# Optimization experiments

Measured on AMD Instinct MI355X. Metric: run time of the kernel, lower is better.

## Reference

```python
import jax, jax.numpy as jnp
import numpy as np

M0, M1 = 32, 16          # multiplicities of 0e (scalars) and 1o (vectors)
FEAT = M0 + 3 * M1       # 80
WNUM = M0*M0 + M1*M1 + M0*M1 + M1*M0  # 2304 per-edge TP weights
N_NODES, N_EDGES, N_RBF, HID = 10000, 160000, 50, 64
EPS = 1e-5
INV_SQRT3 = 1.0 / np.sqrt(3.0)
# per-path normalization: 1/sqrt(num_paths_to_output * mul_in)
A_P1 = 1.0 / np.sqrt(2.0 * M0)   # 0e x 0e -> 0e
A_P4 = 1.0 / np.sqrt(2.0 * M1)   # 1o x 1o -> 0e
A_P2 = 1.0 / np.sqrt(2.0 * M1)   # 1o x 0e -> 1o
A_P3 = 1.0 / np.sqrt(2.0 * M0)   # 0e x 1o -> 1o


def setup_inputs() -> dict:
    key = jax.random.key(0)
    ks = jax.random.split(key, 12)
    def lin(k, fi, fo):
        return jax.random.normal(k, (fi, fo), jnp.float32) / np.sqrt(fi)
    return dict(
        h=jax.random.normal(ks[0], (N_NODES, FEAT), jnp.float32),
        edge_index=jax.random.randint(ks[1], (2, N_EDGES), 0, N_NODES),
        edge_sh=jax.random.normal(ks[2], (N_EDGES, 4), jnp.float32),
        edge_features=jax.random.normal(ks[3], (N_EDGES, N_RBF), jnp.float32),
        W1e=lin(ks[4], N_RBF, HID), b1e=jnp.zeros(HID, jnp.float32),
        W2e=lin(ks[5], HID, HID), b2e=jnp.zeros(HID, jnp.float32),
        W3e=lin(ks[6], HID, WNUM) * 0.1, b3e=jnp.zeros(WNUM, jnp.float32),
        A0=jax.random.normal(ks[7], (M0, M0), jnp.float32),
        A1p=jax.random.normal(ks[8], (M1, M1), jnp.float32),
        bn_w0=jnp.ones(M0, jnp.float32), bn_b0=jnp.zeros(M0, jnp.float32),
        bn_w1=jnp.ones(M1, jnp.float32),
    )


def _forward(h, edge_index, edge_sh, edge_features,
             W1e, b1e, W2e, b2e, W3e, b3e, A0, A1p, bn_w0, bn_b0, bn_w1):
    N = h.shape[0]
    E = edge_sh.shape[0]
    src, dst = edge_index[0], edge_index[1]

    # ---- edge MLP -> per-edge tensor-product weights [E, WNUM] ----
    w = jax.nn.silu(edge_features @ W1e + b1e)
    w = jax.nn.silu(w @ W2e + b2e)
    w = w @ W3e + b3e
    o1 = M0 * M0
    o2 = o1 + M1 * M1
    o3 = o2 + M0 * M1
    w1 = w[:, :o1].reshape(E, M0, M0)     # 0e x 0e -> 0e
    w2 = w[:, o1:o2].reshape(E, M1, M1)   # 1o x 0e -> 1o
    w3 = w[:, o2:o3].reshape(E, M0, M1)   # 0e x 1o -> 1o
    w4 = w[:, o3:].reshape(E, M1, M0)     # 1o x 1o -> 0e

    # ---- gather source node features ----
    s0 = h[src, :M0]                         # [E, M0]
    s1 = h[src, M0:].reshape(E, M1, 3)       # [E, M1, 3]
    y0 = edge_sh[:, 0]                       # [E]
    y1 = edge_sh[:, 1:4]                     # [E, 3]

    # ---- fully connected tensor product with per-edge weights ----
    # scalar output: 0e x 0e -> 0e  and  1o x 1o -> 0e (dot / sqrt(3))
    dot11 = jnp.einsum('eui,ei->eu', s1, y1) * INV_SQRT3      # [E, M1]
    m0 = (A_P1 * jnp.einsum('eu,euw->ew', s0 * y0[:, None], w1)
          + A_P4 * jnp.einsum('eu,euw->ew', dot11, w4))       # [E, M0]
    # vector output: 1o x 0e -> 1o  and  0e x 1o -> 1o
    m1 = (A_P2 * jnp.einsum('eui,euw->ewi', s1 * y0[:, None, None], w2)
          + A_P3 * jnp.einsum('eu,ei,euw->ewi', s0, y1, w3))  # [E, M1, 3]
    messages = jnp.concatenate([m0, m1.reshape(E, 3 * M1)], axis=1)  # [E, FEAT]

    # ---- scatter-mean aggregation to destination nodes ----
    agg = jax.ops.segment_sum(messages, dst, num_segments=N)
    cnt = jax.ops.segment_sum(jnp.ones((E,), messages.dtype), dst, num_segments=N)
    agg = agg / jnp.maximum(cnt, 1.0)[:, None]

    # ---- equivariant self-interaction (per-l linear mixing) ----
    self0 = (h[:, :M0] @ A0) / np.sqrt(M0)
    h1 = h[:, M0:].reshape(N, M1, 3)
    self1 = jnp.einsum('nui,uw->nwi', h1, A1p) / np.sqrt(M1)
    out = agg + jnp.concatenate([self0, self1.reshape(N, 3 * M1)], axis=1)

    # ---- equivariant batch norm (layer mode) ----
    x0 = out[:, :M0]
    x1 = out[:, M0:].reshape(N, M1, 3)
    mu = x0.mean(axis=0)
    var = x0.var(axis=0)
    x0n = (x0 - mu) * jax.lax.rsqrt(var + EPS) * bn_w0 + bn_b0
    nrm2 = (x1 ** 2).sum(axis=-1).mean(axis=0)               # [M1]
    x1n = x1 * (jax.lax.rsqrt(nrm2 + EPS) * bn_w1)[None, :, None]
    out = jnp.concatenate([x0n, x1n.reshape(N, 3 * M1)], axis=1)

    # ---- residual (irreps_in == irreps_out) ----
    return out + h


def reference(h, edge_index, edge_sh, edge_features,
              W1e, b1e, W2e, b2e, W3e, b3e, A0, A1p, bn_w0, bn_b0, bn_w1):
    return _forward(h, edge_index, edge_sh, edge_features,
                    W1e, b1e, W2e, b2e, W3e, b3e, A0, A1p, bn_w0, bn_b0, bn_w1)
```

## Files before the change

### kernel.cpp

```cpp
#include <hip/hip_runtime.h>
#include <math.h>

#define NN 10000
#define NE 160000
#define NRBF 50
#define WNUM 2304
#define EPSV 1e-5f

#define A_P1 0.125f
#define A_P2 0.17677669529663687f
#define A_P3 0.125f
#define A_P4 0.17677669529663687f
#define INV_SQRT3 0.5773502691896258f
#define INV_SQRT_M0 0.17677669529663687f
#define INV_SQRT_M1 0.25f

typedef __attribute__((ext_vector_type(8))) short bf16x8;
typedef __attribute__((ext_vector_type(4))) float f32x4;
typedef __attribute__((ext_vector_type(4))) int i32x4;

#define MFMA16(a, b, c) __builtin_amdgcn_mfma_f32_16x16x32_bf16(a, b, c, 0, 0, 0)

__device__ __forceinline__ short f2bf(float x) {
  unsigned u = __float_as_uint(x);
  unsigned r = (u + 0x7fffu + ((u >> 16) & 1u)) >> 16;
  return (short)r;
}

__global__ void prep_weights(const float* __restrict__ W1, const float* __restrict__ W2,
                             const float* __restrict__ W3, short* __restrict__ W1P,
                             short* __restrict__ W2P, short* __restrict__ W3P) {
  int s = blockIdx.x * 256 + threadIdx.x;
  if (s < WNUM * 64) {
    int t = s >> 10, r = s & 1023;
    int ch = r >> 9, l = (r >> 3) & 63, kk = r & 7;
    int row = t * 16 + (l & 15);
    int k = ((l >> 4) << 3) + (ch << 5) + kk;
    W3P[s] = f2bf(W3[k * WNUM + row]);
  } else if (s < WNUM * 64 + 4096) {
    int s2 = s - WNUM * 64;
    int t = s2 >> 10, r = s2 & 1023;
    int ch = r >> 9, l = (r >> 3) & 63, kk = r & 7;
    int row = t * 16 + (l & 15);
    int k = ((l >> 4) << 3) + (ch << 5) + kk;
    W1P[s2] = f2bf(k < NRBF ? W1[k * 64 + row] : 0.f);
  } else if (s < WNUM * 64 + 8192) {
    int s2 = s - WNUM * 64 - 4096;
    int t = s2 >> 10, r = s2 & 1023;
    int ch = r >> 9, l = (r >> 3) & 63, kk = r & 7;
    int row = t * 16 + (l & 15);
    int k = ((l >> 4) << 3) + (ch << 5) + kk;
    W2P[s2] = f2bf(W2[k * 64 + row]);
  }
}

#define TILE_V(JT, V)                                         \
  {                                                           \
    const short* wb = W3P + ((JT) << 10) + (l << 3);          \
    bf16x8 b0 = *(const bf16x8*)wb;                           \
    bf16x8 b1f = *(const bf16x8*)(wb + 512);                  \
    float bias = b3[((JT) << 4) + lr];                        \
    f32x4 d = {bias, bias, bias, bias};                       \
    d = MFMA16(a0, b0, d);                                    \
    V = MFMA16(a1, b1f, d);                                   \
  }

__global__ __launch_bounds__(256, 3) void edge_kernel(
    const float* __restrict__ h, const int* __restrict__ eidx,
    const float* __restrict__ esh, const float* __restrict__ ef,
    const short* __restrict__ W1P, const float* __restrict__ b1,
    const short* __restrict__ W2P, const float* __restrict__ b2,
    const short* __restrict__ W3P, const float* __restrict__ b3,
    float* __restrict__ agg, float* __restrict__ cnt) {
  __shared__ short buf0[64 * 72];
  __shared__ short h1s[64 * 72];
  __shared__ float a0s[32 * 64];
  __shared__ float s0c[32 * 64];
  __shared__ float cYs[3 * 16 * 64];
  __shared__ float d4s[16 * 64];
  __shared__ float y1s[3 * 64];
  __shared__ float b1s[64], b2s[64];
  __shared__ int dsts[64];

  const int tid = threadIdx.x;
  const int e0 = blockIdx.x * 64;

  for (int idx = tid; idx < 64 * 64; idx += 256) {
    int e = idx >> 6, k = idx & 63;
    float v = (k < NRBF) ? ef[(long)(e0 + e) * NRBF + k] : 0.f;
    buf0[e * 72 + k] = f2bf(v);
  }
  if (tid < 64) { b1s[tid] = b1[tid]; b2s[tid] = b2[tid]; }
  {
    int e = tid >> 2, q = tid & 3;
    int ge = e0 + e;
    int src = eidx[ge];
    float y0 = esh[ge * 4 + 0];
    float y1x = esh[ge * 4 + 1], y1y = esh[ge * 4 + 2], y1z = esh[ge * 4 + 3];
    const float* hs = h + (long)src * 80;
    for (int u = q; u < 32; u += 4) {
      float s = hs[u];
      a0s[u * 64 + e] = A_P1 * y0 * s;
      s0c[u * 64 + e] = A_P3 * s;
    }
    for (int u = q; u < 16; u += 4) {
      float sx = hs[32 + u * 3], sy = hs[33 + u * 3], sz = hs[34 + u * 3];
      cYs[(0 * 16 + u) * 64 + e] = A_P2 * y0 * sx;
      cYs[(1 * 16 + u) * 64 + e] = A_P2 * y0 * sy;
      cYs[(2 * 16 + u) * 64 + e] = A_P2 * y0 * sz;
      d4s[u * 64 + e] = A_P4 * INV_SQRT3 * (sx * y1x + sy * y1y + sz * y1z);
    }
    if (q == 0) {
      y1s[0 * 64 + e] = y1x; y1s[1 * 64 + e] = y1y; y1s[2 * 64 + e] = y1z;
      dsts[e] = eidx[NE + ge];
    }
  }
  __syncthreads();

  const int wid = tid >> 6, l = tid & 63;
  const int er = wid * 16;
  const int lr = l & 15, lg = l >> 4;
  const int row4 = er + lg * 4;

  {
    bf16x8 a0 = *(const bf16x8*)&buf0[(er + lr) * 72 + lg * 8];
    bf16x8 a1 = *(const bf16x8*)&buf0[(er + lr) * 72 + 32 + lg * 8];
#pragma unroll
    for (int jt = 0; jt < 4; ++jt) {
      const short* wb = W1P + (jt << 10) + (l << 3);
      bf16x8 b0 = *(const bf16x8*)wb;
      bf16x8 b1f = *(const bf16x8*)(wb + 512);
      float bias = b1s[jt * 16 + lr];
      f32x4 d = {bias, bias, bias, bias};
      d = MFMA16(a0, b0, d);
      d = MFMA16(a1, b1f, d);
#pragma unroll
      for (int r = 0; r < 4; ++r) {
        float x = d[r];
        x = x / (1.f + __expf(-x));
        h1s[(row4 + r) * 72 + jt * 16 + lr] = f2bf(x);
      }
    }
  }
  __syncthreads();

  {
    bf16x8 a0 = *(const bf16x8*)&h1s[(er + lr) * 72 + lg * 8];
    bf16x8 a1 = *(const bf16x8*)&h1s[(er + lr) * 72 + 32 + lg * 8];
#pragma unroll
    for (int jt = 0; jt < 4; ++jt) {
      const short* wb = W2P + (jt << 10) + (l << 3);
      bf16x8 b0 = *(const bf16x8*)wb;
      bf16x8 b1f = *(const bf16x8*)(wb + 512);
      float bias = b2s[jt * 16 + lr];
      f32x4 d = {bias, bias, bias, bias};
      d = MFMA16(a0, b0, d);
      d = MFMA16(a1, b1f, d);
#pragma unroll
      for (int r = 0; r < 4; ++r) {
        float x = d[r];
        x = x / (1.f + __expf(-x));
        buf0[(row4 + r) * 72 + jt * 16 + lr] = f2bf(x);
      }
    }
  }
  __syncthreads();

  bf16x8 a0 = *(const bf16x8*)&buf0[(er + lr) * 72 + lg * 8];
  bf16x8 a1 = *(const bf16x8*)&buf0[(er + lr) * 72 + 32 + lg * 8];
  f32x4 y1r0 = *(const f32x4*)&y1s[0 * 64 + row4];
  f32x4 y1r1 = *(const f32x4*)&y1s[1 * 64 + row4];
  f32x4 y1r2 = *(const f32x4*)&y1s[2 * 64 + row4];
  i32x4 dd = *(const i32x4*)&dsts[row4];

  f32x4 m0f0 = {0.f, 0.f, 0.f, 0.f}, m0f1 = {0.f, 0.f, 0.f, 0.f};
  f32x4 m1f0 = {0.f, 0.f, 0.f, 0.f}, m1f1 = {0.f, 0.f, 0.f, 0.f},
        m1f2 = {0.f, 0.f, 0.f, 0.f};

#pragma unroll 2
  for (int jp = 0; jp < 32; ++jp) {
    f32x4 c = *(const f32x4*)&a0s[jp * 64 + row4];
    f32x4 v, v2;
    TILE_V(jp * 2, v);
    TILE_V(jp * 2 + 1, v2);
#pragma unroll
    for (int r = 0; r < 4; ++r) {
      m0f0[r] += c[r] * v[r];
      m0f1[r] += c[r] * v2[r];
    }
  }

#pragma unroll 4
  for (int u = 0; u < 16; ++u) {
    f32x4 v;
    TILE_V(64 + u, v);
    f32x4 c0 = *(const f32x4*)&cYs[(0 * 16 + u) * 64 + row4];
    f32x4 c1 = *(const f32x4*)&cYs[(1 * 16 + u) * 64 + row4];
    f32x4 c2 = *(const f32x4*)&cYs[(2 * 16 + u) * 64 + row4];
#pragma unroll
    for (int r = 0; r < 4; ++r) {
      m1f0[r] += c0[r] * v[r];
      m1f1[r] += c1[r] * v[r];
      m1f2[r] += c2[r] * v[r];
    }
  }

#pragma unroll 4
  for (int u = 0; u < 32; ++u) {
    f32x4 v;
    TILE_V(80 + u, v);
    f32x4 c = *(const f32x4*)&s0c[u * 64 + row4];
#pragma unroll
    for (int r = 0; r < 4; ++r) {
      float t = c[r] * v[r];
      m1f0[r] += t * y1r0[r];
      m1f1[r] += t * y1r1[r];
      m1f2[r] += t * y1r2[r];
    }
  }

#pragma unroll 2
  for (int up = 0; up < 16; ++up) {
    f32x4 c = *(const f32x4*)&d4s[up * 64 + row4];
    f32x4 v, v2;
    TILE_V(112 + up * 2, v);
    TILE_V(112 + up * 2 + 1, v2);
#pragma unroll
    for (int r = 0; r < 4; ++r) {
      m0f0[r] += c[r] * v[r];
      m0f1[r] += c[r] * v2[r];
    }
  }

#pragma unroll
  for (int r = 0; r < 4; ++r) {
    float* base = agg + (long)dd[r] * 80;
    atomicAdd(base + lr, m0f0[r]);
    atomicAdd(base + 16 + lr, m0f1[r]);
    atomicAdd(base + 32 + lr * 3 + 0, m1f0[r]);
    atomicAdd(base + 32 + lr * 3 + 1, m1f1[r]);
    atomicAdd(base + 32 + lr * 3 + 2, m1f2[r]);
  }
  if (tid < 64) atomicAdd(cnt + dsts[tid], 1.0f);
}

__global__ __launch_bounds__(256) void node_a(
    const float* __restrict__ h, const float* __restrict__ A0,
    const float* __restrict__ A1p, const float* __restrict__ agg,
    const float* __restrict__ cnt, float* __restrict__ outpre,
    float* __restrict__ stats) {
  __shared__ float redw[4][80];
  const int tid = threadIdx.x;
  const int wid = tid >> 6, l = tid & 63;
  const int n = blockIdx.x * 256 + tid;
  float x0[32], x1[48];
#pragma unroll
  for (int w = 0; w < 32; w++) x0[w] = 0.f;
#pragma unroll
  for (int c = 0; c < 48; c++) x1[c] = 0.f;
  if (n < NN) {
    const float* hr = h + (long)n * 80;
    const float* ar = agg + (long)n * 80;
    float inv = 1.f / fmaxf(cnt[n], 1.f);
#pragma unroll 1
    for (int u = 0; u < 32; u++) {
      float hu = hr[u];
#pragma unroll
      for (int w = 0; w < 32; w++) x0[w] += hu * A0[u * 32 + w];
    }
#pragma unroll
    for (int w = 0; w < 32; w++) x0[w] = x0[w] * INV_SQRT_M0 + ar[w] * inv;
#pragma unroll 1
    for (int u = 0; u < 16; u++) {
      float a = hr[32 + u * 3], b_ = hr[33 + u * 3], c_ = hr[34 + u * 3];
#pragma unroll
      for (int w = 0; w < 16; w++) {
        float Aw = A1p[u * 16 + w];
        x1[w * 3 + 0] += a * Aw;
        x1[w * 3 + 1] += b_ * Aw;
        x1[w * 3 + 2] += c_ * Aw;
      }
    }
#pragma unroll
    for (int c = 0; c < 48; c++) x1[c] = x1[c] * INV_SQRT_M1 + ar[32 + c] * inv;
    float* opr = outpre + (long)n * 80;
#pragma unroll
    for (int w = 0; w < 32; w++) opr[w] = x0[w];
#pragma unroll
    for (int c = 0; c < 48; c++) opr[32 + c] = x1[c];
  }
#pragma unroll 1
  for (int c = 0; c < 32; ++c) {
    float s = x0[c];
#pragma unroll
    for (int m = 32; m >= 1; m >>= 1) s += __shfl_xor(s, m, 64);
    if (l == 0) redw[wid][c] = s;
  }
#pragma unroll 1
  for (int c = 0; c < 32; ++c) {
    float v = x0[c];
    float s = v * v;
#pragma unroll
    for (int m = 32; m >= 1; m >>= 1) s += __shfl_xor(s, m, 64);
    if (l == 0) redw[wid][32 + c] = s;
  }
#pragma unroll 1
  for (int u = 0; u < 16; ++u) {
    float s = x1[u * 3] * x1[u * 3] + x1[u * 3 + 1] * x1[u * 3 + 1] +
              x1[u * 3 + 2] * x1[u * 3 + 2];
#pragma unroll
    for (int m = 32; m >= 1; m >>= 1) s += __shfl_xor(s, m, 64);
    if (l == 0) redw[wid][64 + u] = s;
  }
  __syncthreads();
  if (tid < 80)
    atomicAdd(&stats[tid],
              redw[0][tid] + redw[1][tid] + redw[2][tid] + redw[3][tid]);
}

__global__ void node_b(const float* __restrict__ outpre, const float* __restrict__ stats,
                       const float* __restrict__ bnw0, const float* __restrict__ bnb0,
                       const float* __restrict__ bnw1, const float* __restrict__ h,
                       float* __restrict__ out) {
  int idx = blockIdx.x * 256 + threadIdx.x;
  if (idx >= NN * 80) return;
  int c = idx % 80;
  float v = outpre[idx];
  const float invN = 1.f / NN;
  float o;
  if (c < 32) {
    float mu = stats[c] * invN;
    float var = stats[32 + c] * invN - mu * mu;
    o = (v - mu) * rsqrtf(var + EPSV) * bnw0[c] + bnb0[c];
  } else {
    int u = (c - 32) / 3;
    float nr = stats[64 + u] * invN;
    o = v * rsqrtf(nr + EPSV) * bnw1[u];
  }
  out[idx] = o + h[idx];
}

extern "C" void kernel_launch(void* const* d_in, const int* in_sizes, int n_in,
                              void* d_out, int out_size, void* d_ws, size_t ws_size,
                              hipStream_t stream) {
  const float* h    = (const float*)d_in[0];
  const int*   eidx = (const int*)d_in[1];
  const float* esh  = (const float*)d_in[2];
  const float* ef   = (const float*)d_in[3];
  const float* W1   = (const float*)d_in[4];
  const float* b1   = (const float*)d_in[5];
  const float* W2   = (const float*)d_in[6];
  const float* b2   = (const float*)d_in[7];
  const float* W3   = (const float*)d_in[8];
  const float* b3   = (const float*)d_in[9];
  const float* A0   = (const float*)d_in[10];
  const float* A1p  = (const float*)d_in[11];
  const float* bnw0 = (const float*)d_in[12];
  const float* bnb0 = (const float*)d_in[13];
  const float* bnw1 = (const float*)d_in[14];
  float* out = (float*)d_out;

  float* ws = (float*)d_ws;
  float* agg    = ws;
  float* cnt    = ws + 800000;
  float* stats  = ws + 810000;
  float* outpre = ws + 810080;
  short* W3P    = (short*)(ws + 1610080);
  short* W1P    = W3P + WNUM * 64;
  short* W2P    = W1P + 4096;

  hipMemsetAsync(agg, 0, (size_t)810080 * sizeof(float), stream);

  prep_weights<<<(WNUM * 64 + 8192 + 255) / 256, 256, 0, stream>>>(W1, W2, W3, W1P,
                                                                   W2P, W3P);
  edge_kernel<<<NE / 64, 256, 0, stream>>>(h, eidx, esh, ef, W1P, b1, W2P, b2, W3P, b3,
                                           agg, cnt);
  node_a<<<(NN + 255) / 256, 256, 0, stream>>>(h, A0, A1p, agg, cnt, outpre, stats);
  node_b<<<(NN * 80 + 255) / 256, 256, 0, stream>>>(outpre, stats, bnw0, bnb0, bnw1, h,
                                                    out);
}
```

Measured before the change: 234.7 us.

## Split W3 tiles across wave halves, reuse each B fragment for two edge groups

The third-layer weight tiles are now split between two wave halves. Each wave computes two 16-edge row groups against each loaded W3 fragment, which halves the global weight loads per MFMA. The y0 factor is pulled out of the per-u coefficients and applied after accumulation, which shrinks the shared coefficient arrays into one buffer. The partial sums of the two halves are combined through shared memory with extra barriers. This raises register pressure and adds a reduction step, but cuts redundant weight traffic.

```diff
diff --git a/kernel.cpp b/kernel.cpp
--- a/kernel.cpp
+++ b/kernel.cpp
@@ -54,15 +54,18 @@
   }
 }
 
-#define TILE_V(JT, V)                                         \
+#define TILE_V2(TL, V0, V1)                                   \
   {                                                           \
-    const short* wb = W3P + ((JT) << 10) + (l << 3);          \
+    const short* wb = WB + ((TL) << 10) + (l << 3);           \
     bf16x8 b0 = *(const bf16x8*)wb;                           \
     bf16x8 b1f = *(const bf16x8*)(wb + 512);                  \
-    float bias = b3[((JT) << 4) + lr];                        \
-    f32x4 d = {bias, bias, bias, bias};                       \
-    d = MFMA16(a0, b0, d);                                    \
-    V = MFMA16(a1, b1f, d);                                   \
+    float bias = B3[((TL) << 4) + lr];                        \
+    f32x4 d0 = {bias, bias, bias, bias};                      \
+    f32x4 d1 = {bias, bias, bias, bias};                      \
+    d0 = MFMA16(aA0, b0, d0);                                 \
+    d1 = MFMA16(aB0, b0, d1);                                 \
+    V0 = MFMA16(aA1, b1f, d0);                                \
+    V1 = MFMA16(aB1, b1f, d1);                                \
   }
 
 __global__ __launch_bounds__(256, 3) void edge_kernel(
@@ -74,11 +77,8 @@
     float* __restrict__ agg, float* __restrict__ cnt) {
   __shared__ short buf0[64 * 72];
   __shared__ short h1s[64 * 72];
-  __shared__ float a0s[32 * 64];
-  __shared__ float s0c[32 * 64];
-  __shared__ float cYs[3 * 16 * 64];
-  __shared__ float d4s[16 * 64];
-  __shared__ float y1s[3 * 64];
+  __shared__ float coef[6144];
+  __shared__ float y0s[64], y1s[192];
   __shared__ float b1s[64], b2s[64];
   __shared__ int dsts[64];
 
@@ -98,31 +98,27 @@
     float y0 = esh[ge * 4 + 0];
     float y1x = esh[ge * 4 + 1], y1y = esh[ge * 4 + 2], y1z = esh[ge * 4 + 3];
     const float* hs = h + (long)src * 80;
-    for (int u = q; u < 32; u += 4) {
-      float s = hs[u];
-      a0s[u * 64 + e] = A_P1 * y0 * s;
-      s0c[u * 64 + e] = A_P3 * s;
-    }
+    for (int u = q; u < 32; u += 4) coef[u * 64 + e] = A_P3 * hs[u];
     for (int u = q; u < 16; u += 4) {
       float sx = hs[32 + u * 3], sy = hs[33 + u * 3], sz = hs[34 + u * 3];
-      cYs[(0 * 16 + u) * 64 + e] = A_P2 * y0 * sx;
-      cYs[(1 * 16 + u) * 64 + e] = A_P2 * y0 * sy;
-      cYs[(2 * 16 + u) * 64 + e] = A_P2 * y0 * sz;
-      d4s[u * 64 + e] = A_P4 * INV_SQRT3 * (sx * y1x + sy * y1y + sz * y1z);
+      coef[2048 + (0 * 16 + u) * 64 + e] = A_P2 * sx;
+      coef[2048 + (1 * 16 + u) * 64 + e] = A_P2 * sy;
+      coef[2048 + (2 * 16 + u) * 64 + e] = A_P2 * sz;
+      coef[5120 + u * 64 + e] = A_P4 * INV_SQRT3 * (sx * y1x + sy * y1y + sz * y1z);
     }
     if (q == 0) {
-      y1s[0 * 64 + e] = y1x; y1s[1 * 64 + e] = y1y; y1s[2 * 64 + e] = y1z;
+      y0s[e] = y0;
+      y1s[e] = y1x; y1s[64 + e] = y1y; y1s[128 + e] = y1z;
       dsts[e] = eidx[NE + ge];
     }
   }
   __syncthreads();
 
   const int wid = tid >> 6, l = tid & 63;
-  const int er = wid * 16;
   const int lr = l & 15, lg = l >> 4;
-  const int row4 = er + lg * 4;
 
   {
+    const int er = wid * 16;
     bf16x8 a0 = *(const bf16x8*)&buf0[(er + lr) * 72 + lg * 8];
     bf16x8 a1 = *(const bf16x8*)&buf0[(er + lr) * 72 + 32 + lg * 8];
 #pragma unroll
@@ -138,13 +134,14 @@
       for (int r = 0; r < 4; ++r) {
         float x = d[r];
         x = x / (1.f + __expf(-x));
-        h1s[(row4 + r) * 72 + jt * 16 + lr] = f2bf(x);
+        h1s[(er + lg * 4 + r) * 72 + jt * 16 + lr] = f2bf(x);
       }
     }
   }
   __syncthreads();
 
   {
+    const int er = wid * 16;
     bf16x8 a0 = *(const bf16x8*)&h1s[(er + lr) * 72 + lg * 8];
     bf16x8 a1 = *(const bf16x8*)&h1s[(er + lr) * 72 + 32 + lg * 8];
 #pragma unroll
@@ -160,86 +157,172 @@
       for (int r = 0; r < 4; ++r) {
         float x = d[r];
         x = x / (1.f + __expf(-x));
-        buf0[(row4 + r) * 72 + jt * 16 + lr] = f2bf(x);
-      }
-    }
-  }
-  __syncthreads();
-
-  bf16x8 a0 = *(const bf16x8*)&buf0[(er + lr) * 72 + lg * 8];
-  bf16x8 a1 = *(const bf16x8*)&buf0[(er + lr) * 72 + 32 + lg * 8];
-  f32x4 y1r0 = *(const f32x4*)&y1s[0 * 64 + row4];
-  f32x4 y1r1 = *(const f32x4*)&y1s[1 * 64 + row4];
-  f32x4 y1r2 = *(const f32x4*)&y1s[2 * 64 + row4];
-  i32x4 dd = *(const i32x4*)&dsts[row4];
-
-  f32x4 m0f0 = {0.f, 0.f, 0.f, 0.f}, m0f1 = {0.f, 0.f, 0.f, 0.f};
-  f32x4 m1f0 = {0.f, 0.f, 0.f, 0.f}, m1f1 = {0.f, 0.f, 0.f, 0.f},
-        m1f2 = {0.f, 0.f, 0.f, 0.f};
-
+        buf0[(er + lg * 4 + r) * 72 + jt * 16 + lr] = f2bf(x);
+      }
+    }
+  }
+  __syncthreads();
+
+  const int gpair = wid & 1, half = wid >> 1;
+  const int g0 = gpair * 2;
+  const int rowA = g0 * 16, rowB = (g0 + 1) * 16;
+  const int r4A = rowA + lg * 4, r4B = rowB + lg * 4;
+
+  bf16x8 aA0 = *(const bf16x8*)&buf0[(rowA + lr) * 72 + lg * 8];
+  bf16x8 aA1 = *(const bf16x8*)&buf0[(rowA + lr) * 72 + 32 + lg * 8];
+  bf16x8 aB0 = *(const bf16x8*)&buf0[(rowB + lr) * 72 + lg * 8];
+  bf16x8 aB1 = *(const bf16x8*)&buf0[(rowB + lr) * 72 + 32 + lg * 8];
+  f32x4 y0A = *(const f32x4*)&y0s[r4A];
+  f32x4 y0B = *(const f32x4*)&y0s[r4B];
+
+  const short* WB = W3P + ((half * 72) << 10);
+  const float* B3 = b3 + half * 72 * 16;
+
+  f32x4 s0A = {0,0,0,0}, s1A = {0,0,0,0}, s0B = {0,0,0,0}, s1B = {0,0,0,0};
+  f32x4 mxA = {0,0,0,0}, myA = {0,0,0,0}, mzA = {0,0,0,0};
+  f32x4 mxB = {0,0,0,0}, myB = {0,0,0,0}, mzB = {0,0,0,0};
+
+  if (half == 0) {
 #pragma unroll 2
-  for (int jp = 0; jp < 32; ++jp) {
-    f32x4 c = *(const f32x4*)&a0s[jp * 64 + row4];
-    f32x4 v, v2;
-    TILE_V(jp * 2, v);
-    TILE_V(jp * 2 + 1, v2);
-#pragma unroll
-    for (int r = 0; r < 4; ++r) {
-      m0f0[r] += c[r] * v[r];
-      m0f1[r] += c[r] * v2[r];
-    }
-  }
-
-#pragma unroll 4
-  for (int u = 0; u < 16; ++u) {
-    f32x4 v;
-    TILE_V(64 + u, v);
-    f32x4 c0 = *(const f32x4*)&cYs[(0 * 16 + u) * 64 + row4];
-    f32x4 c1 = *(const f32x4*)&cYs[(1 * 16 + u) * 64 + row4];
-    f32x4 c2 = *(const f32x4*)&cYs[(2 * 16 + u) * 64 + row4];
-#pragma unroll
-    for (int r = 0; r < 4; ++r) {
-      m1f0[r] += c0[r] * v[r];
-      m1f1[r] += c1[r] * v[r];
-      m1f2[r] += c2[r] * v[r];
-    }
-  }
-
-#pragma unroll 4
-  for (int u = 0; u < 32; ++u) {
-    f32x4 v;
-    TILE_V(80 + u, v);
-    f32x4 c = *(const f32x4*)&s0c[u * 64 + row4];
-#pragma unroll
-    for (int r = 0; r < 4; ++r) {
-      float t = c[r] * v[r];
-      m1f0[r] += t * y1r0[r];
-      m1f1[r] += t * y1r1[r];
-      m1f2[r] += t * y1r2[r];
-    }
-  }
-
+    for (int u = 0; u < 32; ++u) {
+      f32x4 cA = *(const f32x4*)&coef[u * 64 + r4A];
+      f32x4 cB = *(const f32x4*)&coef[u * 64 + r4B];
+      f32x4 vA0, vB0, vA1, vB1;
+      TILE_V2(2 * u, vA0, vB0);
+      TILE_V2(2 * u + 1, vA1, vB1);
+#pragma unroll
+      for (int r = 0; r < 4; ++r) {
+        s0A[r] += cA[r] * vA0[r]; s1A[r] += cA[r] * vA1[r];
+        s0B[r] += cB[r] * vB0[r]; s1B[r] += cB[r] * vB1[r];
+      }
+    }
+#pragma unroll
+    for (int r = 0; r < 4; ++r) {
+      s0A[r] *= y0A[r]; s1A[r] *= y0A[r];
+      s0B[r] *= y0B[r]; s1B[r] *= y0B[r];
+    }
 #pragma unroll 2
-  for (int up = 0; up < 16; ++up) {
-    f32x4 c = *(const f32x4*)&d4s[up * 64 + row4];
-    f32x4 v, v2;
-    TILE_V(112 + up * 2, v);
-    TILE_V(112 + up * 2 + 1, v2);
-#pragma unroll
-    for (int r = 0; r < 4; ++r) {
-      m0f0[r] += c[r] * v[r];
-      m0f1[r] += c[r] * v2[r];
-    }
-  }
-
-#pragma unroll
-  for (int r = 0; r < 4; ++r) {
-    float* base = agg + (long)dd[r] * 80;
-    atomicAdd(base + lr, m0f0[r]);
-    atomicAdd(base + 16 + lr, m0f1[r]);
-    atomicAdd(base + 32 + lr * 3 + 0, m1f0[r]);
-    atomicAdd(base + 32 + lr * 3 + 1, m1f1[r]);
-    atomicAdd(base + 32 + lr * 3 + 2, m1f2[r]);
+    for (int u = 0; u < 8; ++u) {
+      f32x4 v0, v1;
+      TILE_V2(64 + u, v0, v1);
+      f32x4 cxA = *(const f32x4*)&coef[2048 + (0 * 16 + u) * 64 + r4A];
+      f32x4 cyA = *(const f32x4*)&coef[2048 + (1 * 16 + u) * 64 + r4A];
+      f32x4 czA = *(const f32x4*)&coef[2048 + (2 * 16 + u) * 64 + r4A];
+      f32x4 cxB = *(const f32x4*)&coef[2048 + (0 * 16 + u) * 64 + r4B];
+      f32x4 cyB = *(const f32x4*)&coef[2048 + (1 * 16 + u) * 64 + r4B];
+      f32x4 czB = *(const f32x4*)&coef[2048 + (2 * 16 + u) * 64 + r4B];
+#pragma unroll
+      for (int r = 0; r < 4; ++r) {
+        mxA[r] += cxA[r] * v0[r]; myA[r] += cyA[r] * v0[r]; mzA[r] += czA[r] * v0[r];
+        mxB[r] += cxB[r] * v1[r]; myB[r] += cyB[r] * v1[r]; mzB[r] += czB[r] * v1[r];
+      }
+    }
+#pragma unroll
+    for (int r = 0; r < 4; ++r) {
+      mxA[r] *= y0A[r]; myA[r] *= y0A[r]; mzA[r] *= y0A[r];
+      mxB[r] *= y0B[r]; myB[r] *= y0B[r]; mzB[r] *= y0B[r];
+    }
+  } else {
+#pragma unroll 2
+    for (int u = 8; u < 16; ++u) {
+      f32x4 v0, v1;
+      TILE_V2(u - 8, v0, v1);
+      f32x4 cxA = *(const f32x4*)&coef[2048 + (0 * 16 + u) * 64 + r4A];
+      f32x4 cyA = *(const f32x4*)&coef[2048 + (1 * 16 + u) * 64 + r4A];
+      f32x4 czA = *(const f32x4*)&coef[2048 + (2 * 16 + u) * 64 + r4A];
+      f32x4 cxB = *(const f32x4*)&coef[2048 + (0 * 16 + u) * 64 + r4B];
+      f32x4 cyB = *(const f32x4*)&coef[2048 + (1 * 16 + u) * 64 + r4B];
+      f32x4 czB = *(const f32x4*)&coef[2048 + (2 * 16 + u) * 64 + r4B];
+#pragma unroll
+      for (int r = 0; r < 4; ++r) {
+        mxA[r] += cxA[r] * v0[r]; myA[r] += cyA[r] * v0[r]; mzA[r] += czA[r] * v0[r];
+        mxB[r] += cxB[r] * v1[r]; myB[r] += cyB[r] * v1[r]; mzB[r] += czB[r] * v1[r];
+      }
+    }
+#pragma unroll
+    for (int r = 0; r < 4; ++r) {
+      mxA[r] *= y0A[r]; myA[r] *= y0A[r]; mzA[r] *= y0A[r];
+      mxB[r] *= y0B[r]; myB[r] *= y0B[r]; mzB[r] *= y0B[r];
+    }
+    {
+      f32x4 t3A = {0,0,0,0}, t3B = {0,0,0,0};
+#pragma unroll 2
+      for (int u = 0; u < 32; ++u) {
+        f32x4 v0, v1;
+        TILE_V2(8 + u, v0, v1);
+        f32x4 cA = *(const f32x4*)&coef[u * 64 + r4A];
+        f32x4 cB = *(const f32x4*)&coef[u * 64 + r4B];
+#pragma unroll
+        for (int r = 0; r < 4; ++r) {
+          t3A[r] += cA[r] * v0[r];
+          t3B[r] += cB[r] * v1[r];
+        }
+      }
+      f32x4 yxA = *(const f32x4*)&y1s[0 + r4A], yxB = *(const f32x4*)&y1s[0 + r4B];
+      f32x4 yyA = *(const f32x4*)&y1s[64 + r4A], yyB = *(const f32x4*)&y1s[64 + r4B];
+      f32x4 yzA = *(const f32x4*)&y1s[128 + r4A], yzB = *(const f32x4*)&y1s[128 + r4B];
+#pragma unroll
+      for (int r = 0; r < 4; ++r) {
+        mxA[r] += yxA[r] * t3A[r]; myA[r] += yyA[r] * t3A[r]; mzA[r] += yzA[r] * t3A[r];
+        mxB[r] += yxB[r] * t3B[r]; myB[r] += yyB[r] * t3B[r]; mzB[r] += yzB[r] * t3B[r];
+      }
+    }
+#pragma unroll 2
+    for (int up = 0; up < 16; ++up) {
+      f32x4 cA = *(const f32x4*)&coef[5120 + up * 64 + r4A];
+      f32x4 cB = *(const f32x4*)&coef[5120 + up * 64 + r4B];
+      f32x4 vA0, vB0, vA1, vB1;
+      TILE_V2(40 + 2 * up, vA0, vB0);
+      TILE_V2(41 + 2 * up, vA1, vB1);
+#pragma unroll
+      for (int r = 0; r < 4; ++r) {
+        s0A[r] += cA[r] * vA0[r]; s1A[r] += cA[r] * vA1[r];
+        s0B[r] += cB[r] * vB0[r]; s1B[r] += cB[r] * vB1[r];
+      }
+    }
+  }
+
+  __syncthreads();
+  if (half == 1) {
+    float* wr = coef + gpair * 2624 + l * 41;
+#pragma unroll
+    for (int r = 0; r < 4; ++r) {
+      wr[0 + r] = s0A[r];  wr[4 + r] = s1A[r];
+      wr[8 + r] = mxA[r];  wr[12 + r] = myA[r]; wr[16 + r] = mzA[r];
+      wr[20 + r] = s0B[r]; wr[24 + r] = s1B[r];
+      wr[28 + r] = mxB[r]; wr[32 + r] = myB[r]; wr[36 + r] = mzB[r];
+    }
+  }
+  __syncthreads();
+  if (half == 0) {
+    const float* wr = coef + gpair * 2624 + l * 41;
+#pragma unroll
+    for (int r = 0; r < 4; ++r) {
+      s0A[r] += wr[0 + r];  s1A[r] += wr[4 + r];
+      mxA[r] += wr[8 + r];  myA[r] += wr[12 + r]; mzA[r] += wr[16 + r];
+      s0B[r] += wr[20 + r]; s1B[r] += wr[24 + r];
+      mxB[r] += wr[28 + r]; myB[r] += wr[32 + r]; mzB[r] += wr[36 + r];
+    }
+    i32x4 ddA = *(const i32x4*)&dsts[r4A];
+    i32x4 ddB = *(const i32x4*)&dsts[r4B];
+#pragma unroll
+    for (int r = 0; r < 4; ++r) {
+      float* base = agg + (long)ddA[r] * 80;
+      atomicAdd(base + lr, s0A[r]);
+      atomicAdd(base + 16 + lr, s1A[r]);
+      atomicAdd(base + 32 + lr * 3 + 0, mxA[r]);
+      atomicAdd(base + 32 + lr * 3 + 1, myA[r]);
+      atomicAdd(base + 32 + lr * 3 + 2, mzA[r]);
+    }
+#pragma unroll
+    for (int r = 0; r < 4; ++r) {
+      float* base = agg + (long)ddB[r] * 80;
+      atomicAdd(base + lr, s0B[r]);
+      atomicAdd(base + 16 + lr, s1B[r]);
+      atomicAdd(base + 32 + lr * 3 + 0, mxB[r]);
+      atomicAdd(base + 32 + lr * 3 + 1, myB[r]);
+      atomicAdd(base + 32 + lr * 3 + 2, mzB[r]);
+    }
   }
   if (tid < 64) atomicAdd(cnt + dsts[tid], 1.0f);
 }
```

After: 223.4 us. 4.8% less time.

## Split W3 tile work across waves so each wave reuses B fragments for all edges

Applied to the files above, without the earlier changes.

The W3 tensor-product stage is repartitioned. Previously each wave handled 16 edges and loaded every W3 tile. Now each wave handles a range of weight tiles for all 64 edges, and each loaded B fragment feeds four MFMAs. The y0 scaling is factored out of the coefficients and applied once after accumulation. Partial sums are combined through LDS across waves in several barrier-separated steps, and a single wave then issues the atomics. This cuts the global/L2 traffic for W3 fragment loads per block, at the cost of more registers (20 accumulator vectors), an uneven work split across waves, extra syncs, and serialized atomics.

```diff
diff --git a/kernel.cpp b/kernel.cpp
--- a/kernel.cpp
+++ b/kernel.cpp
@@ -54,15 +54,19 @@
   }
 }
 
-#define TILE_V(JT, V)                                         \
-  {                                                           \
-    const short* wb = W3P + ((JT) << 10) + (l << 3);          \
-    bf16x8 b0 = *(const bf16x8*)wb;                           \
-    bf16x8 b1f = *(const bf16x8*)(wb + 512);                  \
-    float bias = b3[((JT) << 4) + lr];                        \
-    f32x4 d = {bias, bias, bias, bias};                       \
-    d = MFMA16(a0, b0, d);                                    \
-    V = MFMA16(a1, b1f, d);                                   \
+#define TILE4(T, ...)                                               \
+  {                                                                 \
+    const short* _wb = W3P + ((T) << 10) + (l << 3);                \
+    bf16x8 _B0 = *(const bf16x8*)_wb;                               \
+    bf16x8 _B1 = *(const bf16x8*)(_wb + 512);                       \
+    float _bias = b3[((T) << 4) + lr];                              \
+    _Pragma("unroll")                                               \
+    for (int g = 0; g < 4; ++g) {                                   \
+      f32x4 _d = {_bias, _bias, _bias, _bias};                      \
+      _d = MFMA16(a0g[g], _B0, _d);                                 \
+      f32x4 v = MFMA16(a1g[g], _B1, _d);                            \
+      __VA_ARGS__                                                   \
+    }                                                               \
   }
 
 __global__ __launch_bounds__(256, 3) void edge_kernel(
@@ -74,11 +78,8 @@
     float* __restrict__ agg, float* __restrict__ cnt) {
   __shared__ short buf0[64 * 72];
   __shared__ short h1s[64 * 72];
-  __shared__ float a0s[32 * 64];
-  __shared__ float s0c[32 * 64];
-  __shared__ float cYs[3 * 16 * 64];
-  __shared__ float d4s[16 * 64];
-  __shared__ float y1s[3 * 64];
+  __shared__ float coef[6144];
+  __shared__ float y0s[64], y1s[192];
   __shared__ float b1s[64], b2s[64];
   __shared__ int dsts[64];
 
@@ -98,31 +99,28 @@
     float y0 = esh[ge * 4 + 0];
     float y1x = esh[ge * 4 + 1], y1y = esh[ge * 4 + 2], y1z = esh[ge * 4 + 3];
     const float* hs = h + (long)src * 80;
-    for (int u = q; u < 32; u += 4) {
-      float s = hs[u];
-      a0s[u * 64 + e] = A_P1 * y0 * s;
-      s0c[u * 64 + e] = A_P3 * s;
-    }
+    for (int u = q; u < 32; u += 4) coef[u * 64 + e] = A_P3 * hs[u];
     for (int u = q; u < 16; u += 4) {
       float sx = hs[32 + u * 3], sy = hs[33 + u * 3], sz = hs[34 + u * 3];
-      cYs[(0 * 16 + u) * 64 + e] = A_P2 * y0 * sx;
-      cYs[(1 * 16 + u) * 64 + e] = A_P2 * y0 * sy;
-      cYs[(2 * 16 + u) * 64 + e] = A_P2 * y0 * sz;
-      d4s[u * 64 + e] = A_P4 * INV_SQRT3 * (sx * y1x + sy * y1y + sz * y1z);
+      coef[2048 + (0 * 16 + u) * 64 + e] = A_P2 * sx;
+      coef[2048 + (1 * 16 + u) * 64 + e] = A_P2 * sy;
+      coef[2048 + (2 * 16 + u) * 64 + e] = A_P2 * sz;
+      coef[5120 + u * 64 + e] = A_P4 * INV_SQRT3 * (sx * y1x + sy * y1y + sz * y1z);
     }
     if (q == 0) {
-      y1s[0 * 64 + e] = y1x; y1s[1 * 64 + e] = y1y; y1s[2 * 64 + e] = y1z;
+      y0s[e] = y0;
+      y1s[e] = y1x; y1s[64 + e] = y1y; y1s[128 + e] = y1z;
       dsts[e] = eidx[NE + ge];
     }
   }
   __syncthreads();
 
   const int wid = tid >> 6, l = tid & 63;
-  const int er = wid * 16;
   const int lr = l & 15, lg = l >> 4;
-  const int row4 = er + lg * 4;
+  const int g16 = lg * 4;
 
   {
+    const int er = wid * 16;
     bf16x8 a0 = *(const bf16x8*)&buf0[(er + lr) * 72 + lg * 8];
     bf16x8 a1 = *(const bf16x8*)&buf0[(er + lr) * 72 + 32 + lg * 8];
 #pragma unroll
@@ -138,13 +136,14 @@
       for (int r = 0; r < 4; ++r) {
         float x = d[r];
         x = x / (1.f + __expf(-x));
-        h1s[(row4 + r) * 72 + jt * 16 + lr] = f2bf(x);
+        h1s[(er + lg * 4 + r) * 72 + jt * 16 + lr] = f2bf(x);
       }
     }
   }
   __syncthreads();
 
   {
+    const int er = wid * 16;
     bf16x8 a0 = *(const bf16x8*)&h1s[(er + lr) * 72 + lg * 8];
     bf16x8 a1 = *(const bf16x8*)&h1s[(er + lr) * 72 + 32 + lg * 8];
 #pragma unroll
@@ -160,88 +159,210 @@
       for (int r = 0; r < 4; ++r) {
         float x = d[r];
         x = x / (1.f + __expf(-x));
-        buf0[(row4 + r) * 72 + jt * 16 + lr] = f2bf(x);
-      }
-    }
-  }
-  __syncthreads();
-
-  bf16x8 a0 = *(const bf16x8*)&buf0[(er + lr) * 72 + lg * 8];
-  bf16x8 a1 = *(const bf16x8*)&buf0[(er + lr) * 72 + 32 + lg * 8];
-  f32x4 y1r0 = *(const f32x4*)&y1s[0 * 64 + row4];
-  f32x4 y1r1 = *(const f32x4*)&y1s[1 * 64 + row4];
-  f32x4 y1r2 = *(const f32x4*)&y1s[2 * 64 + row4];
-  i32x4 dd = *(const i32x4*)&dsts[row4];
-
-  f32x4 m0f0 = {0.f, 0.f, 0.f, 0.f}, m0f1 = {0.f, 0.f, 0.f, 0.f};
-  f32x4 m1f0 = {0.f, 0.f, 0.f, 0.f}, m1f1 = {0.f, 0.f, 0.f, 0.f},
-        m1f2 = {0.f, 0.f, 0.f, 0.f};
-
+        buf0[(er + lg * 4 + r) * 72 + jt * 16 + lr] = f2bf(x);
+      }
+    }
+  }
+  __syncthreads();
+
+  bf16x8 a0g[4], a1g[4];
+#pragma unroll
+  for (int g = 0; g < 4; ++g) {
+    a0g[g] = *(const bf16x8*)&buf0[(g * 16 + lr) * 72 + lg * 8];
+    a1g[g] = *(const bf16x8*)&buf0[(g * 16 + lr) * 72 + 32 + lg * 8];
+  }
+
+  f32x4 s0[4], s1[4], mx[4], my[4], mz[4];
+#pragma unroll
+  for (int g = 0; g < 4; ++g) {
+    s0[g] = (f32x4){0, 0, 0, 0}; s1[g] = (f32x4){0, 0, 0, 0};
+    mx[g] = (f32x4){0, 0, 0, 0}; my[g] = (f32x4){0, 0, 0, 0};
+    mz[g] = (f32x4){0, 0, 0, 0};
+  }
+
+  if (wid == 0) {
+#pragma unroll 1
+    for (int p = 0; p < 18; ++p) {
+      TILE4(2 * p, {
+        f32x4 c = *(const f32x4*)&coef[p * 64 + g * 16 + g16];
+        _Pragma("unroll") for (int r = 0; r < 4; ++r) s0[g][r] += c[r] * v[r];
+      });
+      TILE4(2 * p + 1, {
+        f32x4 c = *(const f32x4*)&coef[p * 64 + g * 16 + g16];
+        _Pragma("unroll") for (int r = 0; r < 4; ++r) s1[g][r] += c[r] * v[r];
+      });
+    }
+#pragma unroll
+    for (int g = 0; g < 4; ++g) {
+      f32x4 y0v = *(const f32x4*)&y0s[g * 16 + g16];
+#pragma unroll
+      for (int r = 0; r < 4; ++r) { s0[g][r] *= y0v[r]; s1[g][r] *= y0v[r]; }
+    }
+  } else if (wid == 1) {
+#pragma unroll 1
+    for (int p = 18; p < 32; ++p) {
+      TILE4(2 * p, {
+        f32x4 c = *(const f32x4*)&coef[p * 64 + g * 16 + g16];
+        _Pragma("unroll") for (int r = 0; r < 4; ++r) s0[g][r] += c[r] * v[r];
+      });
+      TILE4(2 * p + 1, {
+        f32x4 c = *(const f32x4*)&coef[p * 64 + g * 16 + g16];
+        _Pragma("unroll") for (int r = 0; r < 4; ++r) s1[g][r] += c[r] * v[r];
+      });
+    }
 #pragma unroll 2
-  for (int jp = 0; jp < 32; ++jp) {
-    f32x4 c = *(const f32x4*)&a0s[jp * 64 + row4];
-    f32x4 v, v2;
-    TILE_V(jp * 2, v);
-    TILE_V(jp * 2 + 1, v2);
-#pragma unroll
-    for (int r = 0; r < 4; ++r) {
-      m0f0[r] += c[r] * v[r];
-      m0f1[r] += c[r] * v2[r];
-    }
-  }
-
-#pragma unroll 4
-  for (int u = 0; u < 16; ++u) {
-    f32x4 v;
-    TILE_V(64 + u, v);
-    f32x4 c0 = *(const f32x4*)&cYs[(0 * 16 + u) * 64 + row4];
-    f32x4 c1 = *(const f32x4*)&cYs[(1 * 16 + u) * 64 + row4];
-    f32x4 c2 = *(const f32x4*)&cYs[(2 * 16 + u) * 64 + row4];
-#pragma unroll
-    for (int r = 0; r < 4; ++r) {
-      m1f0[r] += c0[r] * v[r];
-      m1f1[r] += c1[r] * v[r];
-      m1f2[r] += c2[r] * v[r];
-    }
-  }
-
-#pragma unroll 4
-  for (int u = 0; u < 32; ++u) {
-    f32x4 v;
-    TILE_V(80 + u, v);
-    f32x4 c = *(const f32x4*)&s0c[u * 64 + row4];
-#pragma unroll
-    for (int r = 0; r < 4; ++r) {
-      float t = c[r] * v[r];
-      m1f0[r] += t * y1r0[r];
-      m1f1[r] += t * y1r1[r];
-      m1f2[r] += t * y1r2[r];
-    }
-  }
-
+    for (int u = 0; u < 8; ++u) {
+      TILE4(64 + u, {
+        f32x4 cx = *(const f32x4*)&coef[2048 + (0 * 16 + u) * 64 + g * 16 + g16];
+        f32x4 cy = *(const f32x4*)&coef[2048 + (1 * 16 + u) * 64 + g * 16 + g16];
+        f32x4 cz = *(const f32x4*)&coef[2048 + (2 * 16 + u) * 64 + g * 16 + g16];
+        _Pragma("unroll") for (int r = 0; r < 4; ++r) {
+          mx[g][r] += cx[r] * v[r];
+          my[g][r] += cy[r] * v[r];
+          mz[g][r] += cz[r] * v[r];
+        }
+      });
+    }
+#pragma unroll
+    for (int g = 0; g < 4; ++g) {
+      f32x4 y0v = *(const f32x4*)&y0s[g * 16 + g16];
+#pragma unroll
+      for (int r = 0; r < 4; ++r) {
+        s0[g][r] *= y0v[r]; s1[g][r] *= y0v[r];
+        mx[g][r] *= y0v[r]; my[g][r] *= y0v[r]; mz[g][r] *= y0v[r];
+      }
+    }
+  } else if (wid == 2) {
 #pragma unroll 2
-  for (int up = 0; up < 16; ++up) {
-    f32x4 c = *(const f32x4*)&d4s[up * 64 + row4];
-    f32x4 v, v2;
-    TILE_V(112 + up * 2, v);
-    TILE_V(112 + up * 2 + 1, v2);
-#pragma unroll
-    for (int r = 0; r < 4; ++r) {
-      m0f0[r] += c[r] * v[r];
-      m0f1[r] += c[r] * v2[r];
-    }
-  }
-
-#pragma unroll
-  for (int r = 0; r < 4; ++r) {
-    float* base = agg + (long)dd[r] * 80;
-    atomicAdd(base + lr, m0f0[r]);
-    atomicAdd(base + 16 + lr, m0f1[r]);
-    atomicAdd(base + 32 + lr * 3 + 0, m1f0[r]);
-    atomicAdd(base + 32 + lr * 3 + 1, m1f1[r]);
-    atomicAdd(base + 32 + lr * 3 + 2, m1f2[r]);
-  }
+    for (int u = 8; u < 16; ++u) {
+      TILE4(64 + u, {
+        f32x4 cx = *(const f32x4*)&coef[2048 + (0 * 16 + u) * 64 + g * 16 + g16];
+        f32x4 cy = *(const f32x4*)&coef[2048 + (1 * 16 + u) * 64 + g * 16 + g16];
+        f32x4 cz = *(const f32x4*)&coef[2048 + (2 * 16 + u) * 64 + g * 16 + g16];
+        _Pragma("unroll") for (int r = 0; r < 4; ++r) {
+          mx[g][r] += cx[r] * v[r];
+          my[g][r] += cy[r] * v[r];
+          mz[g][r] += cz[r] * v[r];
+        }
+      });
+    }
+#pragma unroll
+    for (int g = 0; g < 4; ++g) {
+      f32x4 y0v = *(const f32x4*)&y0s[g * 16 + g16];
+#pragma unroll
+      for (int r = 0; r < 4; ++r) {
+        mx[g][r] *= y0v[r]; my[g][r] *= y0v[r]; mz[g][r] *= y0v[r];
+      }
+    }
+#pragma unroll 2
+    for (int u = 0; u < 28; ++u) {
+      TILE4(80 + u, {
+        f32x4 c = *(const f32x4*)&coef[u * 64 + g * 16 + g16];
+        _Pragma("unroll") for (int r = 0; r < 4; ++r) s0[g][r] += c[r] * v[r];
+      });
+    }
+#pragma unroll
+    for (int g = 0; g < 4; ++g) {
+      f32x4 yx = *(const f32x4*)&y1s[g * 16 + g16];
+      f32x4 yy = *(const f32x4*)&y1s[64 + g * 16 + g16];
+      f32x4 yz = *(const f32x4*)&y1s[128 + g * 16 + g16];
+#pragma unroll
+      for (int r = 0; r < 4; ++r) {
+        mx[g][r] += yx[r] * s0[g][r];
+        my[g][r] += yy[r] * s0[g][r];
+        mz[g][r] += yz[r] * s0[g][r];
+      }
+      s0[g] = (f32x4){0, 0, 0, 0};
+    }
+  } else {
+    {
+      f32x4 yx[4], yy[4], yz[4];
+#pragma unroll
+      for (int g = 0; g < 4; ++g) {
+        yx[g] = *(const f32x4*)&y1s[g * 16 + g16];
+        yy[g] = *(const f32x4*)&y1s[64 + g * 16 + g16];
+        yz[g] = *(const f32x4*)&y1s[128 + g * 16 + g16];
+      }
+#pragma unroll 2
+      for (int u = 28; u < 32; ++u) {
+        TILE4(80 + u, {
+          f32x4 c = *(const f32x4*)&coef[u * 64 + g * 16 + g16];
+          _Pragma("unroll") for (int r = 0; r < 4; ++r) {
+            float t = c[r] * v[r];
+            mx[g][r] += yx[g][r] * t;
+            my[g][r] += yy[g][r] * t;
+            mz[g][r] += yz[g][r] * t;
+          }
+        });
+      }
+    }
+#pragma unroll 1
+    for (int p = 0; p < 16; ++p) {
+      TILE4(112 + 2 * p, {
+        f32x4 c = *(const f32x4*)&coef[5120 + p * 64 + g * 16 + g16];
+        _Pragma("unroll") for (int r = 0; r < 4; ++r) s0[g][r] += c[r] * v[r];
+      });
+      TILE4(113 + 2 * p, {
+        f32x4 c = *(const f32x4*)&coef[5120 + p * 64 + g * 16 + g16];
+        _Pragma("unroll") for (int r = 0; r < 4; ++r) s1[g][r] += c[r] * v[r];
+      });
+    }
+  }
+
   if (tid < 64) atomicAdd(cnt + dsts[tid], 1.0f);
+
+#define STORE_G(G, BASE)                                \
+  {                                                     \
+    float* p = coef + (BASE) + l * 24;                  \
+    *(f32x4*)(p + 0) = s0[G];  *(f32x4*)(p + 4) = s1[G];\
+    *(f32x4*)(p + 8) = mx[G];  *(f32x4*)(p + 12) = my[G];\
+    *(f32x4*)(p + 16) = mz[G];                          \
+  }
+#define ADD_G(G, BASE)                                                   \
+  {                                                                      \
+    const float* p = coef + (BASE) + l * 24;                             \
+    f32x4 t0 = *(const f32x4*)(p + 0), t1 = *(const f32x4*)(p + 4);      \
+    f32x4 t2 = *(const f32x4*)(p + 8), t3_ = *(const f32x4*)(p + 12);    \
+    f32x4 t4 = *(const f32x4*)(p + 16);                                  \
+    _Pragma("unroll") for (int r = 0; r < 4; ++r) {                      \
+      s0[G][r] += t0[r]; s1[G][r] += t1[r]; mx[G][r] += t2[r];           \
+      my[G][r] += t3_[r]; mz[G][r] += t4[r];                             \
+    }                                                                    \
+  }
+
+  __syncthreads();
+  if (wid == 1) { STORE_G(0, 0); STORE_G(1, 1536); }
+  if (wid == 3) { STORE_G(0, 3072); STORE_G(1, 4608); }
+  __syncthreads();
+  if (wid == 0) { ADD_G(0, 0); ADD_G(1, 1536); }
+  if (wid == 2) { ADD_G(0, 3072); ADD_G(1, 4608); }
+  __syncthreads();
+  if (wid == 1) { STORE_G(2, 0); STORE_G(3, 1536); }
+  if (wid == 3) { STORE_G(2, 3072); STORE_G(3, 4608); }
+  __syncthreads();
+  if (wid == 0) { ADD_G(2, 0); ADD_G(3, 1536); }
+  if (wid == 2) { ADD_G(2, 3072); ADD_G(3, 4608); }
+  __syncthreads();
+  if (wid == 2) { STORE_G(0, 0); STORE_G(1, 1536); STORE_G(2, 3072); STORE_G(3, 4608); }
+  __syncthreads();
+  if (wid == 0) {
+    ADD_G(0, 0); ADD_G(1, 1536); ADD_G(2, 3072); ADD_G(3, 4608);
+#pragma unroll
+    for (int g = 0; g < 4; ++g) {
+      i32x4 dd = *(const i32x4*)&dsts[g * 16 + g16];
+#pragma unroll
+      for (int r = 0; r < 4; ++r) {
+        float* base = agg + (long)dd[r] * 80;
+        atomicAdd(base + lr, s0[g][r]);
+        atomicAdd(base + 16 + lr, s1[g][r]);
+        atomicAdd(base + 32 + lr * 3 + 0, mx[g][r]);
+        atomicAdd(base + 32 + lr * 3 + 1, my[g][r]);
+        atomicAdd(base + 32 + lr * 3 + 2, mz[g][r]);
+      }
+    }
+  }
+#undef STORE_G
+#undef ADD_G
 }
 
 __global__ __launch_bounds__(256) void node_a(
```

Measured after the change: 235.4 us. About the same (+0.3%).
